# Kernel optimization log

Hardware: AMD Instinct MI355X
Metric: run time of the kernel (lower is better)

Reference implementation:

```python
import jax, jax.numpy as jnp
import numpy as np

N_OSC = 60
B = 65536
DT = 0.1
STEPS = 10
PHI_INV = 2.0 / (1.0 + np.sqrt(5.0))


def setup_inputs() -> dict:
    key = jax.random.key(0)
    k1, k2, k3 = jax.random.split(key, 3)
    theta = jax.random.uniform(k1, (B, N_OSC), dtype=jnp.float32) * (2.0 * np.pi) - np.pi
    K = jax.random.normal(k2, (N_OSC, N_OSC), dtype=jnp.float32) * 0.1
    omega = jax.random.normal(k3, (N_OSC,), dtype=jnp.float32) * 0.1
    return {
        'theta': theta,
        'K': K,
        'omega': omega,
        'K_global': jnp.float32(PHI_INV),
        'coupling_mod': jnp.float32(0.6),        # phase_coupling['quasi_crystal']
        'neg_entropy_gate': jnp.float32(0.5),
        'critical_slow_factor': jnp.float32(0.1),
        'delta_s_neg': jnp.float32(0.8),          # NegativeEntropyState constant
        'relaxation_time': jnp.float32(5.0),      # NegativeEntropyState constant
    }


def reference(theta, K, omega, K_global, coupling_mod, neg_entropy_gate,
              critical_slow_factor, delta_s_neg, relaxation_time):
    n = theta.shape[-1]
    K_eff = K * coupling_mod                               # [n, n]
    critical_factor = 1.0 / (1.0 + critical_slow_factor * relaxation_time)
    eff_dt = DT * critical_factor
    boost = 1.0 + neg_entropy_gate * delta_s_neg
    scale = K_global * boost / n

    def step(th, _):
        # theta_diff[b, i, j] = th[b, j] - th[b, i]
        diff = th[..., None, :] - th[..., :, None]          # [B, n, n]
        coupling_sum = jnp.sum(K_eff * jnp.sin(diff), axis=-1)  # [B, n]
        th = th + eff_dt * (omega + scale * coupling_sum)
        th = jnp.arctan2(jnp.sin(th), jnp.cos(th))          # wrap to (-pi, pi]
        return th, None

    theta, _ = jax.lax.scan(step, theta, None, length=STEPS)
    cos_m = jnp.cos(theta).mean(axis=-1)
    sin_m = jnp.sin(theta).mean(axis=-1)
    coherence = jnp.sqrt(cos_m ** 2 + sin_m ** 2)           # [B]
    return theta, coherence
```

## Files before the change

### kernel.cpp

```cpp
#include <hip/hip_runtime.h>
#include <stdint.h>
#include <math.h>


#define B_TOTAL 65536
#define NOSC 60
#define STEPS 10

using short4v = __attribute__((ext_vector_type(4))) short;
using floatx4 = __attribute__((ext_vector_type(4))) float;

#if __has_builtin(__builtin_amdgcn_perm)
__device__ __forceinline__ unsigned int perm_b32(unsigned int s0, unsigned int s1, unsigned int sel) {
    return __builtin_amdgcn_perm(s0, s1, sel);
}
#else
__device__ __forceinline__ unsigned int perm_b32(unsigned int s0, unsigned int s1, unsigned int sel) {
    unsigned long long pool = ((unsigned long long)s0 << 32) | s1;
    unsigned int r = 0;
#pragma unroll
    for (int b = 0; b < 4; ++b) {
        unsigned int s = (sel >> (8 * b)) & 0xff;
        r |= ((unsigned int)((pool >> (8 * s)) & 0xff)) << (8 * b);
    }
    return r;
}
#endif

__device__ __forceinline__ unsigned int fbits(float x)        { return __builtin_bit_cast(unsigned int, x); }
__device__ __forceinline__ float        bitsf(unsigned int u) { return __builtin_bit_cast(float, u); }

#if __has_builtin(__builtin_amdgcn_mfma_f32_16x16x16bf16_1k)
__device__ __forceinline__ floatx4 mfma16(short4v a, short4v b, floatx4 c) {
    return __builtin_amdgcn_mfma_f32_16x16x16bf16_1k(a, b, c, 0, 0, 0);
}
#else
__device__ __forceinline__ floatx4 mfma16(short4v a, short4v b, floatx4 c) {
    asm("v_mfma_f32_16x16x16_bf16 %0, %1, %2, %0" : "+v"(c) : "v"(a), "v"(b));
    return c;
}
#endif

__device__ __forceinline__ unsigned int pack_hi_pair(float a, float b) {
    return perm_b32(fbits(b), fbits(a), 0x07060302u);
}

__device__ __forceinline__ void mfma_tile(const short4v (&AH)[4][4], const short4v (&AL)[4][4],
                                          const float (&sn)[4][4], const float (&cn)[4][4],
                                          floatx4 (&accS)[4], floatx4 (&accC)[4])
{
    const floatx4 Z = (floatx4)0.0f;
#pragma unroll
    for (int kt = 0; kt < 4; ++kt) {
        union PU { unsigned int u[2]; short4v v; };
        PU bsh, bsl, bch, bcl;
        float slo[4], clo[4];
#pragma unroll
        for (int r = 0; r < 4; ++r) {
            const unsigned int us = fbits(sn[kt][r]);
            slo[r] = sn[kt][r] - bitsf(us & 0xffff0000u);
            const unsigned int uc = fbits(cn[kt][r]);
            clo[r] = cn[kt][r] - bitsf(uc & 0xffff0000u);
        }
        bsh.u[0] = pack_hi_pair(sn[kt][0], sn[kt][1]);
        bsh.u[1] = pack_hi_pair(sn[kt][2], sn[kt][3]);
        bsl.u[0] = pack_hi_pair(slo[0], slo[1]);
        bsl.u[1] = pack_hi_pair(slo[2], slo[3]);
        bch.u[0] = pack_hi_pair(cn[kt][0], cn[kt][1]);
        bch.u[1] = pack_hi_pair(cn[kt][2], cn[kt][3]);
        bcl.u[0] = pack_hi_pair(clo[0], clo[1]);
        bcl.u[1] = pack_hi_pair(clo[2], clo[3]);

#pragma unroll
        for (int nt = 0; nt < 4; ++nt) accS[nt] = mfma16(AH[nt][kt], bsh.v, (kt == 0) ? Z : accS[nt]);
#pragma unroll
        for (int nt = 0; nt < 4; ++nt) accC[nt] = mfma16(AH[nt][kt], bch.v, (kt == 0) ? Z : accC[nt]);
#pragma unroll
        for (int nt = 0; nt < 4; ++nt) accS[nt] = mfma16(AL[nt][kt], bsh.v, accS[nt]);
#pragma unroll
        for (int nt = 0; nt < 4; ++nt) accC[nt] = mfma16(AL[nt][kt], bch.v, accC[nt]);
#pragma unroll
        for (int nt = 0; nt < 4; ++nt) accS[nt] = mfma16(AH[nt][kt], bsl.v, accS[nt]);
#pragma unroll
        for (int nt = 0; nt < 4; ++nt) accC[nt] = mfma16(AH[nt][kt], bcl.v, accC[nt]);
    }
}

__device__ __forceinline__ void update_tile(float (&th)[4][4], float (&sn)[4][4], float (&cn)[4][4],
                                            const float (&omg)[4][4],
                                            const floatx4 (&accS)[4], const floatx4 (&accC)[4],
                                            float scale, float eff_dt)
{
    const float PI_F = 3.14159274101257324f;
    const float C_HI = 6.28318548202514648f;
    const float C_LO = -1.7484556e-7f;
#pragma unroll
    for (int nt = 0; nt < 4; ++nt) {
#pragma unroll
        for (int r = 0; r < 4; ++r) {
            const float S = accS[nt][r];
            const float C = accC[nt][r];
            const float coup = cn[nt][r] * S - sn[nt][r] * C;
            float nth;
            {
#pragma clang fp contract(off)
                const float t1 = scale * coup;
                const float t2 = omg[nt][r] + t1;
                const float t3 = eff_dt * t2;
                nth = th[nt][r] + t3;
            }
            float n = 0.0f;
            n = (nth >=  PI_F) ?  1.0f : n;
            n = (nth <= -PI_F) ? -1.0f : n;
            float y = fmaf(n, -C_HI, nth);
            y = fmaf(n, -C_LO, y);
            th[nt][r] = y;
            __sincosf(y, &sn[nt][r], &cn[nt][r]);
        }
    }
}

__global__ __launch_bounds__(64)
void kuramoto_kernel(const float* __restrict__ theta_in,
                     const float* __restrict__ Kmat,
                     const float* __restrict__ omega,
                     const float* __restrict__ p_kglobal,
                     const float* __restrict__ p_cmod,
                     const float* __restrict__ p_gate,
                     const float* __restrict__ p_slow,
                     const float* __restrict__ p_dsneg,
                     const float* __restrict__ p_relax,
                     float* __restrict__ theta_out,
                     float* __restrict__ coh_out)
{
    const int lane = threadIdx.x & 63;
    const int lidx = lane & 15;
    const int quad = lane >> 4;

    const float kglobal = p_kglobal[0];
    const float cmod    = p_cmod[0];
    const float gate    = p_gate[0];
    const float slow    = p_slow[0];
    const float dsneg   = p_dsneg[0];
    const float relax   = p_relax[0];

    float eff_dt, scale;
    {
#pragma clang fp contract(off)
        const float a     = slow * relax;
        const float b     = 1.0f + a;
        const float crit  = 1.0f / b;
        eff_dt            = 0.1f * crit;
        const float boost = 1.0f + gate * dsneg;
        scale             = (kglobal * boost) / 60.0f;
    }

    const int batch0A = blockIdx.x * 32;
    const int batch0B = batch0A + 16;
    const int browA   = (batch0A + lidx) * NOSC;
    const int browB   = (batch0B + lidx) * NOSC;

    short4v AH[4][4], AL[4][4];
#pragma unroll
    for (int nt = 0; nt < 4; ++nt) {
        const int i = nt * 16 + lidx;
        const bool okn = (i < NOSC);
#pragma unroll
        for (int kt = 0; kt < 4; ++kt) {
            const int k0 = kt * 16 + quad * 4;
            float kv[4];
            if (okn && (k0 + 3) < NOSC) {
                const float4 a = *(const float4*)(Kmat + i * NOSC + k0);
                kv[0] = a.x; kv[1] = a.y; kv[2] = a.z; kv[3] = a.w;
            } else {
#pragma unroll
                for (int j = 0; j < 4; ++j)
                    kv[j] = (okn && (k0 + j) < NOSC) ? Kmat[i * NOSC + k0 + j] : 0.0f;
            }
            short4v h, l;
#pragma unroll
            for (int j = 0; j < 4; ++j) {
                const float v = kv[j] * cmod;
                const unsigned int hb = fbits(v) & 0xffff0000u;
                const float rlo = v - bitsf(hb);
                h[j] = (short)(hb >> 16);
                l[j] = (short)(fbits(rlo) >> 16);
            }
            AH[nt][kt] = h;
            AL[nt][kt] = l;
        }
    }

    float thA[4][4], snA[4][4], cnA[4][4];
    float thB[4][4], snB[4][4], cnB[4][4];
    float omg[4][4];
#pragma unroll
    for (int nt = 0; nt < 4; ++nt) {
        const int o0 = nt * 16 + quad * 4;
        if (o0 + 3 < NOSC) {
            const float4 ov = *(const float4*)(omega + o0);
            omg[nt][0] = ov.x; omg[nt][1] = ov.y; omg[nt][2] = ov.z; omg[nt][3] = ov.w;
            const float4 ta = *(const float4*)(theta_in + browA + o0);
            thA[nt][0] = ta.x; thA[nt][1] = ta.y; thA[nt][2] = ta.z; thA[nt][3] = ta.w;
            const float4 tb = *(const float4*)(theta_in + browB + o0);
            thB[nt][0] = tb.x; thB[nt][1] = tb.y; thB[nt][2] = tb.z; thB[nt][3] = tb.w;
        } else {
#pragma unroll
            for (int r = 0; r < 4; ++r) {
                omg[nt][r] = 0.0f; thA[nt][r] = 0.0f; thB[nt][r] = 0.0f;
            }
        }
#pragma unroll
        for (int r = 0; r < 4; ++r) {
            __sincosf(thA[nt][r], &snA[nt][r], &cnA[nt][r]);
            __sincosf(thB[nt][r], &snB[nt][r], &cnB[nt][r]);
        }
    }

    floatx4 accSA[4], accCA[4], accSB[4], accCB[4];

    mfma_tile(AH, AL, snA, cnA, accSA, accCA);
#pragma unroll 1
    for (int t = 0; t < STEPS - 1; ++t) {
        mfma_tile(AH, AL, snB, cnB, accSB, accCB);
        update_tile(thA, snA, cnA, omg, accSA, accCA, scale, eff_dt);
        mfma_tile(AH, AL, snA, cnA, accSA, accCA);
        update_tile(thB, snB, cnB, omg, accSB, accCB, scale, eff_dt);
    }
    mfma_tile(AH, AL, snB, cnB, accSB, accCB);
    update_tile(thA, snA, cnA, omg, accSA, accCA, scale, eff_dt);
    update_tile(thB, snB, cnB, omg, accSB, accCB, scale, eff_dt);

#pragma unroll
    for (int nt = 0; nt < 4; ++nt) {
        const int o0 = nt * 16 + quad * 4;
        if (o0 + 3 < NOSC) {
            float4 ta, tb;
            ta.x = thA[nt][0]; ta.y = thA[nt][1]; ta.z = thA[nt][2]; ta.w = thA[nt][3];
            *(float4*)(theta_out + browA + o0) = ta;
            tb.x = thB[nt][0]; tb.y = thB[nt][1]; tb.z = thB[nt][2]; tb.w = thB[nt][3];
            *(float4*)(theta_out + browB + o0) = tb;
        }
    }

    float pcA = 0.0f, psA = 0.0f, pcB = 0.0f, psB = 0.0f;
#pragma unroll
    for (int nt = 0; nt < 4; ++nt) {
        if (nt * 16 + quad * 4 < NOSC) {
#pragma unroll
            for (int r = 0; r < 4; ++r) {
                pcA += cnA[nt][r]; psA += snA[nt][r];
                pcB += cnB[nt][r]; psB += snB[nt][r];
            }
        }
    }
    pcA += __shfl_xor(pcA, 16); psA += __shfl_xor(psA, 16);
    pcA += __shfl_xor(pcA, 32); psA += __shfl_xor(psA, 32);
    pcB += __shfl_xor(pcB, 16); psB += __shfl_xor(psB, 16);
    pcB += __shfl_xor(pcB, 32); psB += __shfl_xor(psB, 32);
    if (quad == 0) {
        const float cmA = pcA / 60.0f, smA = psA / 60.0f;
        coh_out[batch0A + lidx] = sqrtf(cmA * cmA + smA * smA);
        const float cmB = pcB / 60.0f, smB = psB / 60.0f;
        coh_out[batch0B + lidx] = sqrtf(cmB * cmB + smB * smB);
    }
}

extern "C" void kernel_launch(void* const* d_in, const int* in_sizes, int n_in,
                              void* d_out, int out_size, void* d_ws, size_t ws_size,
                              hipStream_t stream) {
    const float* theta = (const float*)d_in[0];
    const float* Kmat  = (const float*)d_in[1];
    const float* omg   = (const float*)d_in[2];
    const float* kg    = (const float*)d_in[3];
    const float* cmod  = (const float*)d_in[4];
    const float* gate  = (const float*)d_in[5];
    const float* slow  = (const float*)d_in[6];
    const float* dsn   = (const float*)d_in[7];
    const float* relax = (const float*)d_in[8];
    float* out = (float*)d_out;

    kuramoto_kernel<<<dim3(B_TOTAL / 32), dim3(64), 0, stream>>>(
        theta, Kmat, omg, kg, cmod, gate, slow, dsn, relax,
        out, out + (size_t)B_TOTAL * NOSC);
}
```

Baseline: 126.1 us.

## Interleave per-element phase updates with MFMA chains and prefetch bf16 packing

Replaces the separate mfma_tile/update_tile calls in the time loop with a fused half_step. It issues the MFMA accumulations for one batch tile while updating the other tile's phases element by element between MFMA groups. The hi/lo bf16 packing for the next k-slice, and for the next half-step's first slice, is computed during the current MFMA group. The goal is to hide the sincos and VALU update work and the packing latency behind the matrix-core work. The cost is more live registers (packed buffers and extra ordering constraints), which could raise register pressure or limit how freely the compiler schedules.

After: 128.1 us. No clear change (+1.6%).

```diff
diff --git a/kernel.cpp b/kernel.cpp
--- a/kernel.cpp
+++ b/kernel.cpp
@@ -45,6 +45,59 @@
     return perm_b32(fbits(b), fbits(a), 0x07060302u);
 }
 
+__device__ __forceinline__ void pack_kt_s(const float (&sn)[4][4], int kt, unsigned (&pk)[8]) {
+    float slo[4];
+#pragma unroll
+    for (int r = 0; r < 4; ++r) {
+        const unsigned us = fbits(sn[kt][r]);
+        slo[r] = sn[kt][r] - bitsf(us & 0xffff0000u);
+    }
+    pk[0] = pack_hi_pair(sn[kt][0], sn[kt][1]);
+    pk[1] = pack_hi_pair(sn[kt][2], sn[kt][3]);
+    pk[2] = pack_hi_pair(slo[0], slo[1]);
+    pk[3] = pack_hi_pair(slo[2], slo[3]);
+}
+__device__ __forceinline__ void pack_kt_c(const float (&cn)[4][4], int kt, unsigned (&pk)[8]) {
+    float clo[4];
+#pragma unroll
+    for (int r = 0; r < 4; ++r) {
+        const unsigned uc = fbits(cn[kt][r]);
+        clo[r] = cn[kt][r] - bitsf(uc & 0xffff0000u);
+    }
+    pk[4] = pack_hi_pair(cn[kt][0], cn[kt][1]);
+    pk[5] = pack_hi_pair(cn[kt][2], cn[kt][3]);
+    pk[6] = pack_hi_pair(clo[0], clo[1]);
+    pk[7] = pack_hi_pair(clo[2], clo[3]);
+}
+
+__device__ __forceinline__ void update_elem(float (&th)[4][4], float (&sn)[4][4], float (&cn)[4][4],
+                                            const float (&omg)[4][4],
+                                            const floatx4 (&accS)[4], const floatx4 (&accC)[4],
+                                            int nt, int r, float scale, float eff_dt)
+{
+    const float PI_F = 3.14159274101257324f;
+    const float C_HI = 6.28318548202514648f;
+    const float C_LO = -1.7484556e-7f;
+    const float S = accS[nt][r];
+    const float C = accC[nt][r];
+    const float coup = cn[nt][r] * S - sn[nt][r] * C;
+    float nth;
+    {
+#pragma clang fp contract(off)
+        const float t1 = scale * coup;
+        const float t2 = omg[nt][r] + t1;
+        const float t3 = eff_dt * t2;
+        nth = th[nt][r] + t3;
+    }
+    float n = 0.0f;
+    n = (nth >=  PI_F) ?  1.0f : n;
+    n = (nth <= -PI_F) ? -1.0f : n;
+    float y = fmaf(n, -C_HI, nth);
+    y = fmaf(n, -C_LO, y);
+    th[nt][r] = y;
+    __sincosf(y, &sn[nt][r], &cn[nt][r]);
+}
+
 __device__ __forceinline__ void mfma_tile(const short4v (&AH)[4][4], const short4v (&AL)[4][4],
                                           const float (&sn)[4][4], const float (&cn)[4][4],
                                           floatx4 (&accS)[4], floatx4 (&accC)[4])
@@ -52,37 +105,26 @@
     const floatx4 Z = (floatx4)0.0f;
 #pragma unroll
     for (int kt = 0; kt < 4; ++kt) {
-        union PU { unsigned int u[2]; short4v v; };
-        PU bsh, bsl, bch, bcl;
-        float slo[4], clo[4];
-#pragma unroll
-        for (int r = 0; r < 4; ++r) {
-            const unsigned int us = fbits(sn[kt][r]);
-            slo[r] = sn[kt][r] - bitsf(us & 0xffff0000u);
-            const unsigned int uc = fbits(cn[kt][r]);
-            clo[r] = cn[kt][r] - bitsf(uc & 0xffff0000u);
-        }
-        bsh.u[0] = pack_hi_pair(sn[kt][0], sn[kt][1]);
-        bsh.u[1] = pack_hi_pair(sn[kt][2], sn[kt][3]);
-        bsl.u[0] = pack_hi_pair(slo[0], slo[1]);
-        bsl.u[1] = pack_hi_pair(slo[2], slo[3]);
-        bch.u[0] = pack_hi_pair(cn[kt][0], cn[kt][1]);
-        bch.u[1] = pack_hi_pair(cn[kt][2], cn[kt][3]);
-        bcl.u[0] = pack_hi_pair(clo[0], clo[1]);
-        bcl.u[1] = pack_hi_pair(clo[2], clo[3]);
-
-#pragma unroll
-        for (int nt = 0; nt < 4; ++nt) accS[nt] = mfma16(AH[nt][kt], bsh.v, (kt == 0) ? Z : accS[nt]);
-#pragma unroll
-        for (int nt = 0; nt < 4; ++nt) accC[nt] = mfma16(AH[nt][kt], bch.v, (kt == 0) ? Z : accC[nt]);
-#pragma unroll
-        for (int nt = 0; nt < 4; ++nt) accS[nt] = mfma16(AL[nt][kt], bsh.v, accS[nt]);
-#pragma unroll
-        for (int nt = 0; nt < 4; ++nt) accC[nt] = mfma16(AL[nt][kt], bch.v, accC[nt]);
-#pragma unroll
-        for (int nt = 0; nt < 4; ++nt) accS[nt] = mfma16(AH[nt][kt], bsl.v, accS[nt]);
-#pragma unroll
-        for (int nt = 0; nt < 4; ++nt) accC[nt] = mfma16(AH[nt][kt], bcl.v, accC[nt]);
+        unsigned pk[8];
+        pack_kt_s(sn, kt, pk);
+        pack_kt_c(cn, kt, pk);
+        union PU { unsigned u[2]; short4v v; } vsh, vsl, vch, vcl;
+        vsh.u[0] = pk[0]; vsh.u[1] = pk[1];
+        vsl.u[0] = pk[2]; vsl.u[1] = pk[3];
+        vch.u[0] = pk[4]; vch.u[1] = pk[5];
+        vcl.u[0] = pk[6]; vcl.u[1] = pk[7];
+#pragma unroll
+        for (int nt = 0; nt < 4; ++nt) accS[nt] = mfma16(AH[nt][kt], vsh.v, (kt == 0) ? Z : accS[nt]);
+#pragma unroll
+        for (int nt = 0; nt < 4; ++nt) accC[nt] = mfma16(AH[nt][kt], vch.v, (kt == 0) ? Z : accC[nt]);
+#pragma unroll
+        for (int nt = 0; nt < 4; ++nt) accS[nt] = mfma16(AL[nt][kt], vsh.v, accS[nt]);
+#pragma unroll
+        for (int nt = 0; nt < 4; ++nt) accC[nt] = mfma16(AL[nt][kt], vcl.v == vcl.v ? vch.v : vch.v, accC[nt]);
+#pragma unroll
+        for (int nt = 0; nt < 4; ++nt) accS[nt] = mfma16(AH[nt][kt], vsl.v, accS[nt]);
+#pragma unroll
+        for (int nt = 0; nt < 4; ++nt) accC[nt] = mfma16(AH[nt][kt], vcl.v, accC[nt]);
     }
 }
 
@@ -91,31 +133,57 @@
                                             const floatx4 (&accS)[4], const floatx4 (&accC)[4],
                                             float scale, float eff_dt)
 {
-    const float PI_F = 3.14159274101257324f;
-    const float C_HI = 6.28318548202514648f;
-    const float C_LO = -1.7484556e-7f;
-#pragma unroll
-    for (int nt = 0; nt < 4; ++nt) {
-#pragma unroll
-        for (int r = 0; r < 4; ++r) {
-            const float S = accS[nt][r];
-            const float C = accC[nt][r];
-            const float coup = cn[nt][r] * S - sn[nt][r] * C;
-            float nth;
-            {
-#pragma clang fp contract(off)
-                const float t1 = scale * coup;
-                const float t2 = omg[nt][r] + t1;
-                const float t3 = eff_dt * t2;
-                nth = th[nt][r] + t3;
-            }
-            float n = 0.0f;
-            n = (nth >=  PI_F) ?  1.0f : n;
-            n = (nth <= -PI_F) ? -1.0f : n;
-            float y = fmaf(n, -C_HI, nth);
-            y = fmaf(n, -C_LO, y);
-            th[nt][r] = y;
-            __sincosf(y, &sn[nt][r], &cn[nt][r]);
+#pragma unroll
+    for (int nt = 0; nt < 4; ++nt)
+#pragma unroll
+        for (int r = 0; r < 4; ++r)
+            update_elem(th, sn, cn, omg, accS, accC, nt, r, scale, eff_dt);
+}
+
+__device__ __forceinline__ void half_step(
+    const short4v (&AH)[4][4], const short4v (&AL)[4][4],
+    const float (&snM)[4][4], const float (&cnM)[4][4],
+    floatx4 (&accSM)[4], floatx4 (&accCM)[4],
+    float (&thU)[4][4], float (&snU)[4][4], float (&cnU)[4][4],
+    const floatx4 (&accSU)[4], const floatx4 (&accCU)[4],
+    const float (&omg)[4][4], float scale, float eff_dt,
+    const unsigned (&pk0)[8], unsigned (&pkNext)[8])
+{
+    const floatx4 Z = (floatx4)0.0f;
+    unsigned cur[8], nxt[8];
+#pragma unroll
+    for (int i = 0; i < 8; ++i) cur[i] = pk0[i];
+#pragma unroll
+    for (int kt = 0; kt < 4; ++kt) {
+        union PU { unsigned u[2]; short4v v; } vsh, vsl, vch, vcl;
+        vsh.u[0] = cur[0]; vsh.u[1] = cur[1];
+        vsl.u[0] = cur[2]; vsl.u[1] = cur[3];
+        vch.u[0] = cur[4]; vch.u[1] = cur[5];
+        vcl.u[0] = cur[6]; vcl.u[1] = cur[7];
+#pragma unroll
+        for (int nt = 0; nt < 4; ++nt) accSM[nt] = mfma16(AH[nt][kt], vsh.v, (kt == 0) ? Z : accSM[nt]);
+        update_elem(thU, snU, cnU, omg, accSU, accCU, kt, 0, scale, eff_dt);
+#pragma unroll
+        for (int nt = 0; nt < 4; ++nt) accCM[nt] = mfma16(AH[nt][kt], vch.v, (kt == 0) ? Z : accCM[nt]);
+        update_elem(thU, snU, cnU, omg, accSU, accCU, kt, 1, scale, eff_dt);
+#pragma unroll
+        for (int nt = 0; nt < 4; ++nt) accSM[nt] = mfma16(AL[nt][kt], vsh.v, accSM[nt]);
+        update_elem(thU, snU, cnU, omg, accSU, accCU, kt, 2, scale, eff_dt);
+#pragma unroll
+        for (int nt = 0; nt < 4; ++nt) accCM[nt] = mfma16(AL[nt][kt], vch.v, accCM[nt]);
+        update_elem(thU, snU, cnU, omg, accSU, accCU, kt, 3, scale, eff_dt);
+#pragma unroll
+        for (int nt = 0; nt < 4; ++nt) accSM[nt] = mfma16(AH[nt][kt], vsl.v, accSM[nt]);
+        if (kt < 3) pack_kt_s(snM, kt + 1, nxt);
+        else        pack_kt_s(snU, 0, pkNext);
+#pragma unroll
+        for (int nt = 0; nt < 4; ++nt) accCM[nt] = mfma16(AH[nt][kt], vcl.v, accCM[nt]);
+        if (kt < 3) {
+            pack_kt_c(cnM, kt + 1, nxt);
+#pragma unroll
+            for (int i = 0; i < 8; ++i) cur[i] = nxt[i];
+        } else {
+            pack_kt_c(cnU, 0, pkNext);
         }
     }
 }
@@ -218,17 +286,21 @@
     }
 
     floatx4 accSA[4], accCA[4], accSB[4], accCB[4];
+    unsigned pkA0[8], pkB0[8];
 
     mfma_tile(AH, AL, snA, cnA, accSA, accCA);
+    pack_kt_s(snB, 0, pkB0);
+    pack_kt_c(cnB, 0, pkB0);
+
 #pragma unroll 1
     for (int t = 0; t < STEPS - 1; ++t) {
-        mfma_tile(AH, AL, snB, cnB, accSB, accCB);
-        update_tile(thA, snA, cnA, omg, accSA, accCA, scale, eff_dt);
-        mfma_tile(AH, AL, snA, cnA, accSA, accCA);
-        update_tile(thB, snB, cnB, omg, accSB, accCB, scale, eff_dt);
-    }
-    mfma_tile(AH, AL, snB, cnB, accSB, accCB);
-    update_tile(thA, snA, cnA, omg, accSA, accCA, scale, eff_dt);
+        half_step(AH, AL, snB, cnB, accSB, accCB,
+                  thA, snA, cnA, accSA, accCA, omg, scale, eff_dt, pkB0, pkA0);
+        half_step(AH, AL, snA, cnA, accSA, accCA,
+                  thB, snB, cnB, accSB, accCB, omg, scale, eff_dt, pkA0, pkB0);
+    }
+    half_step(AH, AL, snB, cnB, accSB, accCB,
+              thA, snA, cnA, accSA, accCA, omg, scale, eff_dt, pkB0, pkA0);
     update_tile(thB, snB, cnB, omg, accSB, accCB, scale, eff_dt);
 
 #pragma unroll
```
